# Kernel optimization log

Hardware: AMD Instinct MI355X
Metric: run time of the kernel (lower is better)

Reference implementation:

```python
import jax, jax.numpy as jnp
import numpy as np

B, DIM, H, W = 8, 64, 64, 64
N_EMBED = 512
NNZ = 4          # num_nonzero OMP iterations
REG = 1e-7       # tiny Tikhonov term for the batched normal-equation solves


def batch_omp(X, D, S):
    """Batch OMP: for each signal pick S atoms greedily and solve LS on support.
    X: [N, d] signals, D: [d, K] dictionary with unit-norm atoms.
    Returns dense sparse code [N, K] with <= S nonzeros per row.
    Mathematically equivalent to the incremental-Cholesky Batch_OMP: at each
    step we solve G_II gamma = alpha0_I on the current support I.
    """
    N, K = X.shape[0], D.shape[1]
    G = D.T @ D                 # [K, K] Gram matrix (precomputed once)
    alpha0 = X @ D              # [N, K] initial correlations D^T x
    alpha = alpha0
    idx_cols = []
    gamma = None
    idx = None
    for k in range(S):          # static small loop over sparsity level
        j = jnp.argmax(jnp.abs(alpha), axis=1)                # [N] greedy atom
        idx_cols.append(j)
        idx = jnp.stack(idx_cols, axis=1)                     # [N, k+1]
        G_sub = G[idx[:, :, None], idx[:, None, :]]           # [N, k+1, k+1]
        rhs = jnp.take_along_axis(alpha0, idx, axis=1)        # [N, k+1]
        reg = REG * jnp.eye(k + 1, dtype=G.dtype)
        gamma = jnp.linalg.solve(G_sub + reg, rhs[..., None])[..., 0]  # [N, k+1]
        # residual correlations: alpha = alpha0 - G[:, I] gamma  (G symmetric)
        alpha = alpha0 - jnp.einsum('nak,na->nk', G[idx], gamma)
    code = jnp.zeros((N, K), X.dtype).at[jnp.arange(N)[:, None], idx].set(gamma)
    return code


def setup_inputs() -> dict:
    key = jax.random.key(0)
    kx, kd = jax.random.split(key)
    x = jax.random.normal(kx, (B, DIM, H, W), dtype=jnp.float32)
    dictionary = jax.random.normal(kd, (DIM, N_EMBED), dtype=jnp.float32)
    return {"x": x, "dictionary": dictionary}


def reference(x, dictionary):
    perm = jnp.transpose(x, (0, 2, 3, 1))            # [B, H, W, C]
    flat = perm.reshape(-1, DIM)                     # [N, C], N = B*H*W
    # normalize_dict=True: atoms normalized to unit L2 norm (in-place in torch)
    Dn = dictionary / jnp.linalg.norm(dictionary, axis=0, keepdims=True)
    code = batch_omp(flat, Dn, NNZ)                  # [N, K] (torch keeps [K, N])
    quant = (code @ Dn.T).reshape(perm.shape)        # reconstruction
    diff_enc = jnp.mean((quant - perm) ** 2)
    diff_dict = diff_enc                             # backward_dict=False branch
    # straight-through: perm + (quant - perm).detach() == quant in value
    out = jnp.transpose(quant, (0, 3, 1, 2))         # [B, C, H, W]
    ids = jnp.transpose(code.reshape(B, H, W, N_EMBED), (0, 3, 1, 2))  # [B, K, H, W]
    norm_0 = jnp.sum(code != 0, axis=1).astype(jnp.float32)  # L0 per signal, [N]
    num_steps = jnp.float32(NNZ)
    mean_D = jnp.mean(jnp.abs(Dn))
    mean_Z = jnp.mean(jnp.abs(code))
    norm_Z = jnp.mean(norm_0)
    topk_num = max(1, int(norm_0.shape[0] * 0.01))   # static: 327
    top_percentile = jnp.min(jax.lax.top_k(norm_0, topk_num)[0])
    num_zeros = jnp.sum(norm_0 == 0).astype(jnp.float32)
    return (out, diff_enc, diff_dict, ids, num_steps, mean_D, mean_Z,
            norm_Z, top_percentile, num_zeros)
```

## Files before the change

kernel.cpp:

```cpp
#include <hip/hip_runtime.h>
#include <cstdint>
#include <cstddef>

#define BQ 8
#define CDIM 64
#define HQ 64
#define WQ 64
#define KDIM 512
#define N_SIG 32768
#define S_NNZ 4

#define DIFF_ENC_OFF 2097152
#define DIFF_DICT_OFF 2097153
#define IDS_OFF 2097154
#define NUM_STEPS_OFF 18874370
#define MEAN_D_OFF 18874371
#define MEAN_Z_OFF 18874372
#define NORM_Z_OFF 18874373
#define TOP_PCT_OFF 18874374
#define NUM_ZEROS_OFF 18874375

#define WS_PD 16
#define WS_DN 32
#define WS_DNT 32800
#define WS_G 65568
#define WS_WG 327712
#define WS_WI 458784

typedef float v2f __attribute__((ext_vector_type(2)));

__global__ __launch_bounds__(64) void k_dict(const float* __restrict__ D,
                                             float* __restrict__ Dn,
                                             float* __restrict__ DnT,
                                             float* __restrict__ pd) {
  int tid = threadIdx.x;
  int k = blockIdx.x * 64 + tid;
  float ss = 0.f;
  for (int c = 0; c < CDIM; ++c) {
    float v = D[c * KDIM + k];
    ss = fmaf(v, v, ss);
  }
  float nrm = sqrtf(ss);
  float sabs = 0.f;
  for (int c = 0; c < CDIM; ++c) {
    float v = D[c * KDIM + k] / nrm;
    Dn[c * KDIM + k] = v;
    DnT[k * CDIM + c] = v;
    sabs += fabsf(v);
  }
#pragma unroll
  for (int off = 32; off >= 1; off >>= 1) sabs += __shfl_xor(sabs, off);
  if (tid == 0) pd[blockIdx.x] = sabs;
}

__global__ __launch_bounds__(256) void k_ga(const float* __restrict__ X,
                                            const float* __restrict__ Dn,
                                            float* __restrict__ A0,
                                            float* __restrict__ G,
                                            float* __restrict__ W) {
  __shared__ float Xs[64 * 65];
  __shared__ float Dns[64 * 64];
  int tid = threadIdx.x;
  int w = tid & 63, cq = tid >> 6;
  int ty = tid >> 4, tx = tid & 15;

  if (blockIdx.x < 64) {
    if (blockIdx.x == 0 && tid < 16) ((unsigned int*)W)[tid] = 0u;
    int ti = blockIdx.x >> 3, tj = blockIdx.x & 7;
#pragma unroll
    for (int p = 0; p < 16; ++p) {
      int c = p * 4 + cq;
      Xs[c * 64 + w] = Dn[(size_t)c * KDIM + ti * 64 + w];
      Dns[c * 64 + w] = Dn[(size_t)c * KDIM + tj * 64 + w];
    }
    __syncthreads();
    v2f acc[4][2] = {};
    for (int c = 0; c < 64; ++c) {
      float av[4];
#pragma unroll
      for (int i = 0; i < 4; ++i) av[i] = Xs[c * 64 + ty * 4 + i];
      float4 bv = *(const float4*)&Dns[c * 64 + tx * 4];
      v2f b0 = {bv.x, bv.y}, b1 = {bv.z, bv.w};
#pragma unroll
      for (int i = 0; i < 4; ++i) {
        v2f a2 = {av[i], av[i]};
        acc[i][0] = __builtin_elementwise_fma(a2, b0, acc[i][0]);
        acc[i][1] = __builtin_elementwise_fma(a2, b1, acc[i][1]);
      }
    }
#pragma unroll
    for (int i = 0; i < 4; ++i) {
      float4 st = make_float4(acc[i][0].x, acc[i][0].y, acc[i][1].x, acc[i][1].y);
      *(float4*)&G[(size_t)(ti * 64 + ty * 4 + i) * KDIM + tj * 64 + tx * 4] = st;
    }
  } else {
    int bb = blockIdx.x - 64;
    int mt = bb >> 3, nt = bb & 7;
    int b = mt >> 6, h = mt & 63;
#pragma unroll
    for (int p = 0; p < 16; ++p) {
      int c = p * 4 + cq;
      Xs[w * 65 + c] = X[(((size_t)b * CDIM + c) * HQ + h) * WQ + w];
      Dns[c * 64 + w] = Dn[(size_t)c * KDIM + nt * 64 + w];
    }
    __syncthreads();
    v2f acc[4][2] = {};
    for (int c = 0; c < 64; ++c) {
      float av[4];
#pragma unroll
      for (int i = 0; i < 4; ++i) av[i] = Xs[(ty * 4 + i) * 65 + c];
      float4 bv = *(const float4*)&Dns[c * 64 + tx * 4];
      v2f b0 = {bv.x, bv.y}, b1 = {bv.z, bv.w};
#pragma unroll
      for (int i = 0; i < 4; ++i) {
        v2f a2 = {av[i], av[i]};
        acc[i][0] = __builtin_elementwise_fma(a2, b0, acc[i][0]);
        acc[i][1] = __builtin_elementwise_fma(a2, b1, acc[i][1]);
      }
    }
    size_t n0 = (size_t)mt * 64;
#pragma unroll
    for (int i = 0; i < 4; ++i) {
      float4 st = make_float4(acc[i][0].x, acc[i][0].y, acc[i][1].x, acc[i][1].y);
      *(float4*)&A0[(n0 + ty * 4 + i) * KDIM + nt * 64 + tx * 4] = st;
    }
  }
}

template <int SZ>
__device__ __forceinline__ void solve_sz(const float (&gs)[4][4], const float (&rhs)[4],
                                         float (&gamma)[4]) {
  float M[SZ][SZ];
  float y[SZ];
  float idg[SZ];
#pragma unroll
  for (int a = 0; a < SZ; ++a) {
    y[a] = rhs[a];
#pragma unroll
    for (int b = 0; b < SZ; ++b) M[a][b] = gs[a][b] + (a == b ? 1e-7f : 0.0f);
  }
#pragma unroll
  for (int p = 0; p < SZ; ++p) {
    float ip = __builtin_amdgcn_rcpf(M[p][p]);
    idg[p] = ip;
#pragma unroll
    for (int r = p + 1; r < SZ; ++r) {
      float f = M[r][p] * ip;
#pragma unroll
      for (int c = p + 1; c < SZ; ++c) M[r][c] = fmaf(-f, M[p][c], M[r][c]);
      y[r] = fmaf(-f, y[p], y[r]);
    }
  }
#pragma unroll
  for (int r = SZ - 1; r >= 0; --r) {
    float t = y[r];
#pragma unroll
    for (int c = r + 1; c < SZ; ++c) t = fmaf(-M[r][c], gamma[c], t);
    gamma[r] = t * idg[r];
  }
}

template <int K>
__device__ __forceinline__ void omp_step(int lane, int n, const float* __restrict__ G,
                                         const float* __restrict__ A0,
                                         float (&a0)[8], float (&al)[8], float (&Grow)[3][8],
                                         float (&gs)[4][4], float (&rhs)[4], int (&idx)[4],
                                         float (&gamma)[4]) {
  float mx = fabsf(al[0]);
#pragma unroll
  for (int m = 1; m < 8; ++m) mx = fmaxf(mx, fabsf(al[m]));
#pragma unroll
  for (int off = 32; off >= 1; off >>= 1) mx = fmaxf(mx, __shfl_xor(mx, off));
  int sk = 1 << 30;
#pragma unroll
  for (int m = 0; m < 8; ++m) {
    unsigned long long bm = __ballot(fabsf(al[m]) == mx);
    if (bm) {
      int kk = (int)__builtin_ctzll(bm) * 8 + m;
      sk = kk < sk ? kk : sk;
    }
  }
  idx[K] = sk;

  const float* grow_base = G + (size_t)sk * KDIM;
  if constexpr (K < 3) {
    const float4* gp = (const float4*)(grow_base + lane * 8);
    float4 r0 = gp[0], r1 = gp[1];
    Grow[K][0] = r0.x; Grow[K][1] = r0.y; Grow[K][2] = r0.z; Grow[K][3] = r0.w;
    Grow[K][4] = r1.x; Grow[K][5] = r1.y; Grow[K][6] = r1.z; Grow[K][7] = r1.w;
  }

#pragma unroll
  for (int b = 0; b < K; ++b) {
    float v = grow_base[idx[b]];
    gs[K][b] = v;
    gs[b][K] = v;
  }
  gs[K][K] = grow_base[sk];
  rhs[K] = A0[(size_t)n * KDIM + sk];

  solve_sz<K + 1>(gs, rhs, gamma);

  if constexpr (K < 3) {
#pragma unroll
    for (int m = 0; m < 8; ++m) {
      float acc = a0[m];
#pragma unroll
      for (int a = 0; a <= K; ++a) acc = fmaf(-gamma[a], Grow[a][m], acc);
      al[m] = acc;
    }
  }
}

__global__ __launch_bounds__(256) void k_omp(const float* __restrict__ A0,
                                             const float* __restrict__ G,
                                             float4* __restrict__ wg, int4* __restrict__ wi) {
  int tid = threadIdx.x;
  int lane = tid & 63;
  int wv = __builtin_amdgcn_readfirstlane(tid >> 6);
  int n = blockIdx.x * 4 + wv;
  const float4* ap = (const float4*)(A0 + (size_t)n * KDIM + lane * 8);
  float4 v0 = ap[0], v1 = ap[1];
  float a0[8] = {v0.x, v0.y, v0.z, v0.w, v1.x, v1.y, v1.z, v1.w};
  float al[8];
#pragma unroll
  for (int m = 0; m < 8; ++m) al[m] = a0[m];
  float Grow[3][8];
  float gs[4][4];
  float rhs[4];
  int idx[4];
  float gamma[4];
  omp_step<0>(lane, n, G, A0, a0, al, Grow, gs, rhs, idx, gamma);
  omp_step<1>(lane, n, G, A0, a0, al, Grow, gs, rhs, idx, gamma);
  omp_step<2>(lane, n, G, A0, a0, al, Grow, gs, rhs, idx, gamma);
  omp_step<3>(lane, n, G, A0, a0, al, Grow, gs, rhs, idx, gamma);
  bool k0 = (idx[0] != idx[1]) && (idx[0] != idx[2]) && (idx[0] != idx[3]);
  bool k1 = (idx[1] != idx[2]) && (idx[1] != idx[3]);
  bool k2 = (idx[2] != idx[3]);
  if (lane == 0) {
    wg[n] = make_float4(k0 ? gamma[0] : 0.f, k1 ? gamma[1] : 0.f,
                        k2 ? gamma[2] : 0.f, gamma[3]);
    wi[n] = make_int4(idx[0], idx[1], idx[2], idx[3]);
  }
}

__global__ __launch_bounds__(256) void k_ei(const float* __restrict__ X,
                                            const float* __restrict__ DnT,
                                            const float4* __restrict__ wg,
                                            const int4* __restrict__ wi,
                                            float* __restrict__ out, double* __restrict__ accs,
                                            int* __restrict__ hist) {
  __shared__ __align__(16) int sIdx[64][4];
  __shared__ __align__(16) float sKg[64][4];
  __shared__ float q[64 * 65];
  __shared__ float red[4];
  int tid = threadIdx.x;

  if (blockIdx.x < 512) {
    int bh = blockIdx.x;
    int b = bh >> 6, h = bh & 63;
    if (tid < 64) {
      int w = tid;
      int n = bh * 64 + w;
      int4 iv = wi[n];
      float4 gv = wg[n];
      sIdx[w][0] = iv.x; sIdx[w][1] = iv.y; sIdx[w][2] = iv.z; sIdx[w][3] = iv.w;
      sKg[w][0] = gv.x; sKg[w][1] = gv.y; sKg[w][2] = gv.z; sKg[w][3] = gv.w;
      int nz = (int)(gv.x != 0.f) + (int)(gv.y != 0.f) +
               (int)(gv.z != 0.f) + (int)(gv.w != 0.f);
      float s = fabsf(gv.x) + fabsf(gv.y) + fabsf(gv.z) + fabsf(gv.w);
#pragma unroll
      for (int off = 32; off >= 1; off >>= 1) s += __shfl_xor(s, off);
#pragma unroll
      for (int v = 0; v < 5; ++v) {
        unsigned long long m = __ballot(nz == v);
        if (tid == 0) {
          int c = (int)__popcll(m);
          if (c) atomicAdd(&hist[v], c);
        }
      }
      if (tid == 0) atomicAdd(&accs[0], (double)s);
    }
    __syncthreads();

    int w2 = tid & 63, p = tid >> 6, c0 = p * 16;
    float acc[16] = {};
#pragma unroll
    for (int s = 0; s < 4; ++s) {
      int ks = sIdx[w2][s];
      float g = sKg[w2][s];
      const float4* dp = (const float4*)(DnT + (size_t)ks * CDIM + c0);
#pragma unroll
      for (int i4 = 0; i4 < 4; ++i4) {
        float4 d = dp[i4];
        acc[i4 * 4 + 0] = fmaf(g, d.x, acc[i4 * 4 + 0]);
        acc[i4 * 4 + 1] = fmaf(g, d.y, acc[i4 * 4 + 1]);
        acc[i4 * 4 + 2] = fmaf(g, d.z, acc[i4 * 4 + 2]);
        acc[i4 * 4 + 3] = fmaf(g, d.w, acc[i4 * 4 + 3]);
      }
    }
#pragma unroll
    for (int i = 0; i < 16; ++i) q[(c0 + i) * 65 + w2] = acc[i];
    __syncthreads();

    float sumsq = 0.f;
#pragma unroll
    for (int pass = 0; pass < 16; ++pass) {
      int c = pass * 4 + p;
      float qv = q[c * 65 + w2];
      size_t off = (((size_t)b * CDIM + c) * HQ + h) * WQ + w2;
      float xv = X[off];
      float d = qv - xv;
      sumsq = fmaf(d, d, sumsq);
      out[off] = qv;
    }

#pragma unroll
    for (int off = 32; off >= 1; off >>= 1) sumsq += __shfl_xor(sumsq, off);
    if ((tid & 63) == 0) red[tid >> 6] = sumsq;
    __syncthreads();
    if (tid == 0) atomicAdd(&accs[1], (double)(red[0] + red[1] + red[2] + red[3]));
  } else {
    int bid = blockIdx.x - 512;
    int bh = bid >> 2, kq = bid & 3;
    int b = bh >> 6, h = bh & 63;
    if (tid < 64) {
      int n = bh * 64 + tid;
      *(int4*)&sIdx[tid][0] = wi[n];
      *(float4*)&sKg[tid][0] = wg[n];
    }
    __syncthreads();
    int w = tid & 63, kp = tid >> 6;
    int4 iv = *(int4*)&sIdx[w][0];
    float4 gv = *(float4*)&sKg[w][0];
    int k0 = kq * 128 + kp * 32;
    float* ids = out + IDS_OFF;
    size_t base = (((size_t)b * KDIM + k0) * HQ + h) * WQ + w;
#pragma unroll
    for (int kk = 0; kk < 32; ++kk) {
      int k = k0 + kk;
      float v = 0.f;
      v = (k == iv.x) ? gv.x : v;
      v = (k == iv.y) ? gv.y : v;
      v = (k == iv.z) ? gv.z : v;
      v = (k == iv.w) ? gv.w : v;
      ids[base + (size_t)kk * HQ * WQ] = v;
    }
  }
}

__global__ __launch_bounds__(64) void k_final(const double* __restrict__ accs,
                                              const int* __restrict__ hist,
                                              const float* __restrict__ pd,
                                              float* __restrict__ out) {
  if (threadIdx.x == 0) {
    float sumAbsD = 0.f;
#pragma unroll
    for (int i = 0; i < 8; ++i) sumAbsD += pd[i];
    double sumAbsZ = accs[0], sumSq = accs[1];
    float diff = (float)(sumSq / 2097152.0);
    out[DIFF_ENC_OFF] = diff;
    out[DIFF_DICT_OFF] = diff;
    out[NUM_STEPS_OFF] = 4.0f;
    out[MEAN_D_OFF] = sumAbsD / 32768.0f;
    out[MEAN_Z_OFF] = (float)(sumAbsZ / 16777216.0);
    int h0 = hist[0], h1 = hist[1], h2 = hist[2], h3 = hist[3], h4 = hist[4];
    out[NORM_Z_OFF] = (float)((double)(h1 + 2 * h2 + 3 * h3 + 4 * h4) / 32768.0);
    int cum = 0, res = 0;
    for (int v = 4; v >= 0; --v) {
      cum += hist[v];
      if (cum >= 327) { res = v; break; }
    }
    out[TOP_PCT_OFF] = (float)res;
    out[NUM_ZEROS_OFF] = (float)h0;
  }
}

extern "C" void kernel_launch(void* const* d_in, const int* in_sizes, int n_in,
                              void* d_out, int out_size, void* d_ws, size_t ws_size,
                              hipStream_t stream) {
  (void)in_sizes; (void)n_in; (void)out_size; (void)ws_size;
  const float* X = (const float*)d_in[0];
  const float* D = (const float*)d_in[1];
  float* out = (float*)d_out;
  float* W = (float*)d_ws;
  double* accs = (double*)d_ws;
  int* hist = (int*)W + 4;
  float* pd = W + WS_PD;
  float* Dn = W + WS_DN;
  float* DnT = W + WS_DNT;
  float* G = W + WS_G;
  float4* wgam = (float4*)(W + WS_WG);
  int4* widx = (int4*)(W + WS_WI);
  float* A0 = out;

  hipLaunchKernelGGL(k_dict, dim3(8), dim3(64), 0, stream, D, Dn, DnT, pd);
  hipLaunchKernelGGL(k_ga, dim3(4160), dim3(256), 0, stream, X, Dn, A0, G, W);
  hipLaunchKernelGGL(k_omp, dim3(8192), dim3(256), 0, stream, A0, G, wgam, widx);
  hipLaunchKernelGGL(k_ei, dim3(2560), dim3(256), 0, stream, X, DnT, wgam, widx, out, accs, hist);
  hipLaunchKernelGGL(k_final, dim3(1), dim3(64), 0, stream, accs, hist, pd, out);
}
```

Measured before the change: 171.7 us.

## Use 128x128 register-tiled GEMM on raw dictionary with post-scaling by inverse norms

The Gram and initial-correlation GEMM kernel moves from 64x64 tiles with 4x4 per-thread outputs to 128x128 tiles with 8x8 per-thread outputs, loaded with float4 from global memory. It reads the raw dictionary and applies the inverse atom norms as an epilogue scale, so the normalized copy Dn is no longer written. This cuts the grid from 4160 to 1040 blocks and raises arithmetic intensity. In exchange it uses 64 KB of LDS and more registers per thread, which may lower occupancy, and the results differ from the old ones by rounding.

```diff
diff --git a/kernel.cpp b/kernel.cpp
--- a/kernel.cpp
+++ b/kernel.cpp
@@ -21,17 +21,17 @@
 #define NUM_ZEROS_OFF 18874375
 
 #define WS_PD 16
-#define WS_DN 32
-#define WS_DNT 32800
-#define WS_G 65568
-#define WS_WG 327712
-#define WS_WI 458784
+#define WS_INV 24
+#define WS_DNT 536
+#define WS_G 33304
+#define WS_WG 295448
+#define WS_WI 426520
 
 typedef float v2f __attribute__((ext_vector_type(2)));
 
 __global__ __launch_bounds__(64) void k_dict(const float* __restrict__ D,
-                                             float* __restrict__ Dn,
                                              float* __restrict__ DnT,
+                                             float* __restrict__ invn,
                                              float* __restrict__ pd) {
   int tid = threadIdx.x;
   int k = blockIdx.x * 64 + tid;
@@ -41,10 +41,10 @@
     ss = fmaf(v, v, ss);
   }
   float nrm = sqrtf(ss);
+  invn[k] = 1.0f / nrm;
   float sabs = 0.f;
   for (int c = 0; c < CDIM; ++c) {
     float v = D[c * KDIM + k] / nrm;
-    Dn[c * KDIM + k] = v;
     DnT[k * CDIM + c] = v;
     sabs += fabsf(v);
   }
@@ -54,75 +54,108 @@
 }
 
 __global__ __launch_bounds__(256) void k_ga(const float* __restrict__ X,
-                                            const float* __restrict__ Dn,
+                                            const float* __restrict__ D,
+                                            const float* __restrict__ invn,
                                             float* __restrict__ A0,
                                             float* __restrict__ G,
                                             float* __restrict__ W) {
-  __shared__ float Xs[64 * 65];
-  __shared__ float Dns[64 * 64];
+  __shared__ float As[64 * 128];
+  __shared__ float Bs[64 * 128];
   int tid = threadIdx.x;
-  int w = tid & 63, cq = tid >> 6;
-  int ty = tid >> 4, tx = tid & 15;
-
-  if (blockIdx.x < 64) {
-    if (blockIdx.x == 0 && tid < 16) ((unsigned int*)W)[tid] = 0u;
-    int ti = blockIdx.x >> 3, tj = blockIdx.x & 7;
-#pragma unroll
-    for (int p = 0; p < 16; ++p) {
-      int c = p * 4 + cq;
-      Xs[c * 64 + w] = Dn[(size_t)c * KDIM + ti * 64 + w];
-      Dns[c * 64 + w] = Dn[(size_t)c * KDIM + tj * 64 + w];
-    }
-    __syncthreads();
-    v2f acc[4][2] = {};
-    for (int c = 0; c < 64; ++c) {
-      float av[4];
-#pragma unroll
-      for (int i = 0; i < 4; ++i) av[i] = Xs[c * 64 + ty * 4 + i];
-      float4 bv = *(const float4*)&Dns[c * 64 + tx * 4];
-      v2f b0 = {bv.x, bv.y}, b1 = {bv.z, bv.w};
-#pragma unroll
-      for (int i = 0; i < 4; ++i) {
-        v2f a2 = {av[i], av[i]};
-        acc[i][0] = __builtin_elementwise_fma(a2, b0, acc[i][0]);
-        acc[i][1] = __builtin_elementwise_fma(a2, b1, acc[i][1]);
+  bool gram = blockIdx.x < 16;
+  if (blockIdx.x == 0 && tid < 16) ((unsigned int*)W)[tid] = 0u;
+
+  int nb0, mt = 0, ti = 0;
+  if (gram) {
+    ti = (int)blockIdx.x >> 2;
+    nb0 = ((int)blockIdx.x & 3) * 128;
+  } else {
+    int bb = (int)blockIdx.x - 16;
+    mt = bb >> 2;
+    nb0 = (bb & 3) * 128;
+  }
+
+#pragma unroll
+  for (int p = 0; p < 8; ++p) {
+    int f = tid + p * 256;
+    int c = f >> 5, c4 = (f & 31) * 4;
+    float4 v = *(const float4*)&D[(size_t)c * KDIM + nb0 + c4];
+    *(float4*)&Bs[c * 128 + c4] = v;
+  }
+  if (gram) {
+    int na0 = ti * 128;
+#pragma unroll
+    for (int p = 0; p < 8; ++p) {
+      int f = tid + p * 256;
+      int c = f >> 5, c4 = (f & 31) * 4;
+      float4 v = *(const float4*)&D[(size_t)c * KDIM + na0 + c4];
+      *(float4*)&As[c * 128 + c4] = v;
+    }
+  } else {
+    int b = mt >> 5;
+    int off = (mt & 31) * 128;
+#pragma unroll
+    for (int p = 0; p < 8; ++p) {
+      int f = tid + p * 256;
+      int c = f >> 5, c4 = (f & 31) * 4;
+      float4 v = *(const float4*)&X[((size_t)b * CDIM + c) * 4096 + off + c4];
+      *(float4*)&As[c * 128 + c4] = v;
+    }
+  }
+  __syncthreads();
+
+  int mg = tid >> 4, ng = tid & 15;
+  int m0 = mg * 8, n0 = ng * 8;
+  v2f acc[8][4] = {};
+#pragma unroll 2
+  for (int c = 0; c < 64; ++c) {
+    float4 a0v = *(const float4*)&As[c * 128 + m0];
+    float4 a1v = *(const float4*)&As[c * 128 + m0 + 4];
+    float4 b0v = *(const float4*)&Bs[c * 128 + n0];
+    float4 b1v = *(const float4*)&Bs[c * 128 + n0 + 4];
+    float aa[8] = {a0v.x, a0v.y, a0v.z, a0v.w, a1v.x, a1v.y, a1v.z, a1v.w};
+    v2f bb[4] = {{b0v.x, b0v.y}, {b0v.z, b0v.w}, {b1v.x, b1v.y}, {b1v.z, b1v.w}};
+#pragma unroll
+    for (int i = 0; i < 8; ++i) {
+      v2f ad = {aa[i], aa[i]};
+#pragma unroll
+      for (int j = 0; j < 4; ++j)
+        acc[i][j] = __builtin_elementwise_fma(ad, bb[j], acc[i][j]);
+    }
+  }
+
+  float4 s0 = *(const float4*)&invn[nb0 + n0];
+  float4 s1 = *(const float4*)&invn[nb0 + n0 + 4];
+  float sn[8] = {s0.x, s0.y, s0.z, s0.w, s1.x, s1.y, s1.z, s1.w};
+  if (gram) {
+    int na0 = ti * 128;
+    float4 t0 = *(const float4*)&invn[na0 + m0];
+    float4 t1 = *(const float4*)&invn[na0 + m0 + 4];
+    float sm[8] = {t0.x, t0.y, t0.z, t0.w, t1.x, t1.y, t1.z, t1.w};
+#pragma unroll
+    for (int i = 0; i < 8; ++i) {
+      float r[8];
+#pragma unroll
+      for (int j = 0; j < 4; ++j) {
+        r[2 * j] = acc[i][j].x * sm[i] * sn[2 * j];
+        r[2 * j + 1] = acc[i][j].y * sm[i] * sn[2 * j + 1];
       }
-    }
-#pragma unroll
-    for (int i = 0; i < 4; ++i) {
-      float4 st = make_float4(acc[i][0].x, acc[i][0].y, acc[i][1].x, acc[i][1].y);
-      *(float4*)&G[(size_t)(ti * 64 + ty * 4 + i) * KDIM + tj * 64 + tx * 4] = st;
+      size_t row = (size_t)(na0 + m0 + i) * KDIM + nb0 + n0;
+      *(float4*)&G[row] = make_float4(r[0], r[1], r[2], r[3]);
+      *(float4*)&G[row + 4] = make_float4(r[4], r[5], r[6], r[7]);
     }
   } else {
-    int bb = blockIdx.x - 64;
-    int mt = bb >> 3, nt = bb & 7;
-    int b = mt >> 6, h = mt & 63;
-#pragma unroll
-    for (int p = 0; p < 16; ++p) {
-      int c = p * 4 + cq;
-      Xs[w * 65 + c] = X[(((size_t)b * CDIM + c) * HQ + h) * WQ + w];
-      Dns[c * 64 + w] = Dn[(size_t)c * KDIM + nt * 64 + w];
-    }
-    __syncthreads();
-    v2f acc[4][2] = {};
-    for (int c = 0; c < 64; ++c) {
-      float av[4];
-#pragma unroll
-      for (int i = 0; i < 4; ++i) av[i] = Xs[(ty * 4 + i) * 65 + c];
-      float4 bv = *(const float4*)&Dns[c * 64 + tx * 4];
-      v2f b0 = {bv.x, bv.y}, b1 = {bv.z, bv.w};
-#pragma unroll
-      for (int i = 0; i < 4; ++i) {
-        v2f a2 = {av[i], av[i]};
-        acc[i][0] = __builtin_elementwise_fma(a2, b0, acc[i][0]);
-        acc[i][1] = __builtin_elementwise_fma(a2, b1, acc[i][1]);
+#pragma unroll
+    for (int i = 0; i < 8; ++i) {
+      float r[8];
+#pragma unroll
+      for (int j = 0; j < 4; ++j) {
+        r[2 * j] = acc[i][j].x * sn[2 * j];
+        r[2 * j + 1] = acc[i][j].y * sn[2 * j + 1];
       }
-    }
-    size_t n0 = (size_t)mt * 64;
-#pragma unroll
-    for (int i = 0; i < 4; ++i) {
-      float4 st = make_float4(acc[i][0].x, acc[i][0].y, acc[i][1].x, acc[i][1].y);
-      *(float4*)&A0[(n0 + ty * 4 + i) * KDIM + nt * 64 + tx * 4] = st;
+      size_t row = (size_t)(mt * 128 + m0 + i) * KDIM + nb0 + n0;
+      *(float4*)&A0[row] = make_float4(r[0], r[1], r[2], r[3]);
+      *(float4*)&A0[row + 4] = make_float4(r[4], r[5], r[6], r[7]);
     }
   }
 }
@@ -387,15 +420,15 @@
   double* accs = (double*)d_ws;
   int* hist = (int*)W + 4;
   float* pd = W + WS_PD;
-  float* Dn = W + WS_DN;
+  float* invn = W + WS_INV;
   float* DnT = W + WS_DNT;
   float* G = W + WS_G;
   float4* wgam = (float4*)(W + WS_WG);
   int4* widx = (int4*)(W + WS_WI);
   float* A0 = out;
 
-  hipLaunchKernelGGL(k_dict, dim3(8), dim3(64), 0, stream, D, Dn, DnT, pd);
-  hipLaunchKernelGGL(k_ga, dim3(4160), dim3(256), 0, stream, X, Dn, A0, G, W);
+  hipLaunchKernelGGL(k_dict, dim3(8), dim3(64), 0, stream, D, DnT, invn, pd);
+  hipLaunchKernelGGL(k_ga, dim3(1040), dim3(256), 0, stream, X, D, invn, A0, G, W);
   hipLaunchKernelGGL(k_omp, dim3(8192), dim3(256), 0, stream, A0, G, wgam, widx);
   hipLaunchKernelGGL(k_ei, dim3(2560), dim3(256), 0, stream, X, DnT, wgam, widx, out, accs, hist);
   hipLaunchKernelGGL(k_final, dim3(1), dim3(64), 0, stream, accs, hist, pd, out);
```

After: 174.6 us. About the same (+1.7%).

## Fuse dictionary normalization into GEMM kernel and final reduction into last block

Applied to the files above, without the earlier changes.

Removes the separate dictionary-normalization kernel by computing per-atom inverse norms inside each GEMM block from the raw dictionary and scaling G and A0 outputs afterward; diagonal blocks also write the normalized transpose and abs-sum partials. The final scalar kernel is folded into the expand kernel via a last-block atomic counter. The ids expansion now writes float4 vectors over four pixels per thread. This saves two kernel launches and a serial tiny kernel, at the cost of redundant norm computation per block and slightly different rounding from post-scaling.

```diff
diff --git a/kernel.cpp b/kernel.cpp
--- a/kernel.cpp
+++ b/kernel.cpp
@@ -21,64 +21,79 @@
 #define NUM_ZEROS_OFF 18874375
 
 #define WS_PD 16
-#define WS_DN 32
-#define WS_DNT 32800
-#define WS_G 65568
-#define WS_WG 327712
-#define WS_WI 458784
+#define WS_DNT 24
+#define WS_G 32792
+#define WS_WG 294936
+#define WS_WI 426008
 
 typedef float v2f __attribute__((ext_vector_type(2)));
 
-__global__ __launch_bounds__(64) void k_dict(const float* __restrict__ D,
-                                             float* __restrict__ Dn,
-                                             float* __restrict__ DnT,
-                                             float* __restrict__ pd) {
-  int tid = threadIdx.x;
-  int k = blockIdx.x * 64 + tid;
-  float ss = 0.f;
-  for (int c = 0; c < CDIM; ++c) {
-    float v = D[c * KDIM + k];
-    ss = fmaf(v, v, ss);
-  }
-  float nrm = sqrtf(ss);
-  float sabs = 0.f;
-  for (int c = 0; c < CDIM; ++c) {
-    float v = D[c * KDIM + k] / nrm;
-    Dn[c * KDIM + k] = v;
-    DnT[k * CDIM + c] = v;
-    sabs += fabsf(v);
-  }
-#pragma unroll
-  for (int off = 32; off >= 1; off >>= 1) sabs += __shfl_xor(sabs, off);
-  if (tid == 0) pd[blockIdx.x] = sabs;
-}
-
 __global__ __launch_bounds__(256) void k_ga(const float* __restrict__ X,
-                                            const float* __restrict__ Dn,
+                                            const float* __restrict__ D,
                                             float* __restrict__ A0,
                                             float* __restrict__ G,
+                                            float* __restrict__ DnT,
+                                            float* __restrict__ pd,
                                             float* __restrict__ W) {
   __shared__ float Xs[64 * 65];
   __shared__ float Dns[64 * 64];
+  __shared__ float partA[4][64];
+  __shared__ float partB[4][64];
+  __shared__ float invA[64];
+  __shared__ float invB[64];
   int tid = threadIdx.x;
   int w = tid & 63, cq = tid >> 6;
   int ty = tid >> 4, tx = tid & 15;
+  if (blockIdx.x == 0 && tid < 16) ((unsigned int*)W)[tid] = 0u;
 
   if (blockIdx.x < 64) {
-    if (blockIdx.x == 0 && tid < 16) ((unsigned int*)W)[tid] = 0u;
-    int ti = blockIdx.x >> 3, tj = blockIdx.x & 7;
+    int ti = (int)blockIdx.x >> 3, tj = (int)blockIdx.x & 7;
 #pragma unroll
     for (int p = 0; p < 16; ++p) {
       int c = p * 4 + cq;
-      Xs[c * 64 + w] = Dn[(size_t)c * KDIM + ti * 64 + w];
-      Dns[c * 64 + w] = Dn[(size_t)c * KDIM + tj * 64 + w];
-    }
-    __syncthreads();
+      Xs[c * 64 + w] = D[(size_t)c * KDIM + ti * 64 + w];
+      Dns[c * 64 + w] = D[(size_t)c * KDIM + tj * 64 + w];
+    }
+    __syncthreads();
+    float ssA = 0.f, ssB = 0.f;
+#pragma unroll
+    for (int cc = 0; cc < 16; ++cc) {
+      int c = cq * 16 + cc;
+      float a = Xs[c * 64 + w];
+      ssA = fmaf(a, a, ssA);
+      float bv = Dns[c * 64 + w];
+      ssB = fmaf(bv, bv, ssB);
+    }
+    partA[cq][w] = ssA;
+    partB[cq][w] = ssB;
+    __syncthreads();
+    if (tid < 64) {
+      invA[tid] = 1.0f / sqrtf(partA[0][tid] + partA[1][tid] + partA[2][tid] + partA[3][tid]);
+      invB[tid] = 1.0f / sqrtf(partB[0][tid] + partB[1][tid] + partB[2][tid] + partB[3][tid]);
+    }
+    __syncthreads();
+    if (ti == tj) {
+      int kl = tid >> 2, cp = (tid & 3) * 16;
+      float ia = invA[kl];
+      float sabs = 0.f;
+#pragma unroll
+      for (int i = 0; i < 16; ++i) {
+        int c = cp + i;
+        float v = Xs[c * 64 + kl] * ia;
+        DnT[(size_t)(ti * 64 + kl) * CDIM + c] = v;
+        sabs += fabsf(v);
+      }
+#pragma unroll
+      for (int off = 32; off >= 1; off >>= 1) sabs += __shfl_xor(sabs, off);
+      __syncthreads();
+      if ((tid & 63) == 0) partA[0][tid >> 6] = sabs;
+      __syncthreads();
+      if (tid == 0) pd[ti] = partA[0][0] + partA[0][1] + partA[0][2] + partA[0][3];
+    }
     v2f acc[4][2] = {};
     for (int c = 0; c < 64; ++c) {
-      float av[4];
-#pragma unroll
-      for (int i = 0; i < 4; ++i) av[i] = Xs[c * 64 + ty * 4 + i];
+      float4 avv = *(const float4*)&Xs[c * 64 + ty * 4];
+      float av[4] = {avv.x, avv.y, avv.z, avv.w};
       float4 bv = *(const float4*)&Dns[c * 64 + tx * 4];
       v2f b0 = {bv.x, bv.y}, b1 = {bv.z, bv.w};
 #pragma unroll
@@ -88,21 +103,36 @@
         acc[i][1] = __builtin_elementwise_fma(a2, b1, acc[i][1]);
       }
     }
+    float sn[4] = {invB[tx * 4], invB[tx * 4 + 1], invB[tx * 4 + 2], invB[tx * 4 + 3]};
 #pragma unroll
     for (int i = 0; i < 4; ++i) {
-      float4 st = make_float4(acc[i][0].x, acc[i][0].y, acc[i][1].x, acc[i][1].y);
+      float im = invA[ty * 4 + i];
+      float4 st = make_float4(acc[i][0].x * im * sn[0], acc[i][0].y * im * sn[1],
+                              acc[i][1].x * im * sn[2], acc[i][1].y * im * sn[3]);
       *(float4*)&G[(size_t)(ti * 64 + ty * 4 + i) * KDIM + tj * 64 + tx * 4] = st;
     }
   } else {
-    int bb = blockIdx.x - 64;
+    int bb = (int)blockIdx.x - 64;
     int mt = bb >> 3, nt = bb & 7;
     int b = mt >> 6, h = mt & 63;
 #pragma unroll
     for (int p = 0; p < 16; ++p) {
       int c = p * 4 + cq;
       Xs[w * 65 + c] = X[(((size_t)b * CDIM + c) * HQ + h) * WQ + w];
-      Dns[c * 64 + w] = Dn[(size_t)c * KDIM + nt * 64 + w];
-    }
+      Dns[c * 64 + w] = D[(size_t)c * KDIM + nt * 64 + w];
+    }
+    __syncthreads();
+    float ssB = 0.f;
+#pragma unroll
+    for (int cc = 0; cc < 16; ++cc) {
+      int c = cq * 16 + cc;
+      float bv = Dns[c * 64 + w];
+      ssB = fmaf(bv, bv, ssB);
+    }
+    partB[cq][w] = ssB;
+    __syncthreads();
+    if (tid < 64)
+      invB[tid] = 1.0f / sqrtf(partB[0][tid] + partB[1][tid] + partB[2][tid] + partB[3][tid]);
     __syncthreads();
     v2f acc[4][2] = {};
     for (int c = 0; c < 64; ++c) {
@@ -118,10 +148,12 @@
         acc[i][1] = __builtin_elementwise_fma(a2, b1, acc[i][1]);
       }
     }
+    float sn[4] = {invB[tx * 4], invB[tx * 4 + 1], invB[tx * 4 + 2], invB[tx * 4 + 3]};
     size_t n0 = (size_t)mt * 64;
 #pragma unroll
     for (int i = 0; i < 4; ++i) {
-      float4 st = make_float4(acc[i][0].x, acc[i][0].y, acc[i][1].x, acc[i][1].y);
+      float4 st = make_float4(acc[i][0].x * sn[0], acc[i][0].y * sn[1],
+                              acc[i][1].x * sn[2], acc[i][1].y * sn[3]);
       *(float4*)&A0[(n0 + ty * 4 + i) * KDIM + nt * 64 + tx * 4] = st;
     }
   }
@@ -248,8 +280,11 @@
                                             const float* __restrict__ DnT,
                                             const float4* __restrict__ wg,
                                             const int4* __restrict__ wi,
-                                            float* __restrict__ out, double* __restrict__ accs,
-                                            int* __restrict__ hist) {
+                                            float* __restrict__ out,
+                                            double* __restrict__ accs,
+                                            int* __restrict__ hist,
+                                            int* __restrict__ cnt,
+                                            const float* __restrict__ pd) {
   __shared__ __align__(16) int sIdx[64][4];
   __shared__ __align__(16) float sKg[64][4];
   __shared__ float q[64 * 65];
@@ -330,49 +365,56 @@
       *(float4*)&sKg[tid][0] = wg[n];
     }
     __syncthreads();
-    int w = tid & 63, kp = tid >> 6;
-    int4 iv = *(int4*)&sIdx[w][0];
-    float4 gv = *(float4*)&sKg[w][0];
-    int k0 = kq * 128 + kp * 32;
+    int w4 = (tid & 15) * 4, kl = tid >> 4;
+    int4 I0 = *(const int4*)&sIdx[w4][0];
+    int4 I1 = *(const int4*)&sIdx[w4 + 1][0];
+    int4 I2 = *(const int4*)&sIdx[w4 + 2][0];
+    int4 I3 = *(const int4*)&sIdx[w4 + 3][0];
+    float4 G0 = *(const float4*)&sKg[w4][0];
+    float4 G1 = *(const float4*)&sKg[w4 + 1][0];
+    float4 G2 = *(const float4*)&sKg[w4 + 2][0];
+    float4 G3 = *(const float4*)&sKg[w4 + 3][0];
     float* ids = out + IDS_OFF;
-    size_t base = (((size_t)b * KDIM + k0) * HQ + h) * WQ + w;
-#pragma unroll
-    for (int kk = 0; kk < 32; ++kk) {
-      int k = k0 + kk;
-      float v = 0.f;
-      v = (k == iv.x) ? gv.x : v;
-      v = (k == iv.y) ? gv.y : v;
-      v = (k == iv.z) ? gv.z : v;
-      v = (k == iv.w) ? gv.w : v;
-      ids[base + (size_t)kk * HQ * WQ] = v;
-    }
-  }
-}
-
-__global__ __launch_bounds__(64) void k_final(const double* __restrict__ accs,
-                                              const int* __restrict__ hist,
-                                              const float* __restrict__ pd,
-                                              float* __restrict__ out) {
-  if (threadIdx.x == 0) {
-    float sumAbsD = 0.f;
-#pragma unroll
-    for (int i = 0; i < 8; ++i) sumAbsD += pd[i];
-    double sumAbsZ = accs[0], sumSq = accs[1];
-    float diff = (float)(sumSq / 2097152.0);
-    out[DIFF_ENC_OFF] = diff;
-    out[DIFF_DICT_OFF] = diff;
-    out[NUM_STEPS_OFF] = 4.0f;
-    out[MEAN_D_OFF] = sumAbsD / 32768.0f;
-    out[MEAN_Z_OFF] = (float)(sumAbsZ / 16777216.0);
-    int h0 = hist[0], h1 = hist[1], h2 = hist[2], h3 = hist[3], h4 = hist[4];
-    out[NORM_Z_OFF] = (float)((double)(h1 + 2 * h2 + 3 * h3 + 4 * h4) / 32768.0);
-    int cum = 0, res = 0;
-    for (int v = 4; v >= 0; --v) {
-      cum += hist[v];
-      if (cum >= 327) { res = v; break; }
-    }
-    out[TOP_PCT_OFF] = (float)res;
-    out[NUM_ZEROS_OFF] = (float)h0;
+    size_t base = (((size_t)b * KDIM + kq * 128 + kl) * HQ + h) * WQ + w4;
+#pragma unroll
+    for (int pass = 0; pass < 8; ++pass) {
+      int k = kq * 128 + pass * 16 + kl;
+      float4 v;
+      v.x = (k == I0.w) ? G0.w : (k == I0.z) ? G0.z : (k == I0.y) ? G0.y : (k == I0.x) ? G0.x : 0.f;
+      v.y = (k == I1.w) ? G1.w : (k == I1.z) ? G1.z : (k == I1.y) ? G1.y : (k == I1.x) ? G1.x : 0.f;
+      v.z = (k == I2.w) ? G2.w : (k == I2.z) ? G2.z : (k == I2.y) ? G2.y : (k == I2.x) ? G2.x : 0.f;
+      v.w = (k == I3.w) ? G3.w : (k == I3.z) ? G3.z : (k == I3.y) ? G3.y : (k == I3.x) ? G3.x : 0.f;
+      *(float4*)&ids[base + (size_t)pass * 16 * 4096] = v;
+    }
+  }
+
+  __threadfence();
+  if (tid == 0) {
+    int old = atomicAdd(cnt, 1);
+    if (old == 2559) {
+      float sumAbsD = 0.f;
+#pragma unroll
+      for (int i = 0; i < 8; ++i) sumAbsD += pd[i];
+      double sumAbsZ = atomicAdd(&accs[0], 0.0);
+      double sumSq = atomicAdd(&accs[1], 0.0);
+      int h0 = atomicAdd(&hist[0], 0), h1 = atomicAdd(&hist[1], 0);
+      int h2 = atomicAdd(&hist[2], 0), h3 = atomicAdd(&hist[3], 0);
+      int h4 = atomicAdd(&hist[4], 0);
+      float diff = (float)(sumSq / 2097152.0);
+      out[DIFF_ENC_OFF] = diff;
+      out[DIFF_DICT_OFF] = diff;
+      out[NUM_STEPS_OFF] = 4.0f;
+      out[MEAN_D_OFF] = sumAbsD / 32768.0f;
+      out[MEAN_Z_OFF] = (float)(sumAbsZ / 16777216.0);
+      out[NORM_Z_OFF] = (float)((double)(h1 + 2 * h2 + 3 * h3 + 4 * h4) / 32768.0);
+      int cum = 0, res = 0;
+      for (int v = 4; v >= 0; --v) {
+        cum += hist[v];
+        if (cum >= 327) { res = v; break; }
+      }
+      out[TOP_PCT_OFF] = (float)res;
+      out[NUM_ZEROS_OFF] = (float)h0;
+    }
   }
 }
 
@@ -386,17 +428,16 @@
   float* W = (float*)d_ws;
   double* accs = (double*)d_ws;
   int* hist = (int*)W + 4;
+  int* cnt = (int*)W + 9;
   float* pd = W + WS_PD;
-  float* Dn = W + WS_DN;
   float* DnT = W + WS_DNT;
   float* G = W + WS_G;
   float4* wgam = (float4*)(W + WS_WG);
   int4* widx = (int4*)(W + WS_WI);
   float* A0 = out;
 
-  hipLaunchKernelGGL(k_dict, dim3(8), dim3(64), 0, stream, D, Dn, DnT, pd);
-  hipLaunchKernelGGL(k_ga, dim3(4160), dim3(256), 0, stream, X, Dn, A0, G, W);
+  hipLaunchKernelGGL(k_ga, dim3(4160), dim3(256), 0, stream, X, D, A0, G, DnT, pd, W);
   hipLaunchKernelGGL(k_omp, dim3(8192), dim3(256), 0, stream, A0, G, wgam, widx);
-  hipLaunchKernelGGL(k_ei, dim3(2560), dim3(256), 0, stream, X, DnT, wgam, widx, out, accs, hist);
-  hipLaunchKernelGGL(k_final, dim3(1), dim3(64), 0, stream, accs, hist, pd, out);
-}
+  hipLaunchKernelGGL(k_ei, dim3(2560), dim3(256), 0, stream, X, DnT, wgam, widx, out,
+                     accs, hist, cnt, pd);
+}
```

New measurement: 523.2 us. 3.05x slower.
